# Optimization experiments

Measured on AMD Instinct MI355X. Metric: run time of the kernel, lower is better.

## Reference

```python
import jax, jax.numpy as jnp
import numpy as np

DIM = 384
HEADS = 6
HIDDEN = int(DIM * 4.0)
EPS = 1e-6

def setup_inputs() -> dict:
    key = jax.random.key(0)
    ks = jax.random.split(key, 8)
    s = 0.02
    return {
        "x": jax.random.normal(ks[0], (4, 2048, DIM), dtype=jnp.float32),
        "w_qkv": jax.random.normal(ks[1], (DIM, 3 * DIM), dtype=jnp.float32) * s,
        "b_qkv": jnp.zeros((3 * DIM,), dtype=jnp.float32),
        "w_proj": jax.random.normal(ks[2], (DIM, DIM), dtype=jnp.float32) * s,
        "b_proj": jnp.zeros((DIM,), dtype=jnp.float32),
        "w_fc1": jax.random.normal(ks[3], (DIM, HIDDEN), dtype=jnp.float32) * s,
        "b_fc1": jnp.zeros((HIDDEN,), dtype=jnp.float32),
        "w_fc2": jax.random.normal(ks[4], (HIDDEN, DIM), dtype=jnp.float32) * s,
        "b_fc2": jnp.zeros((DIM,), dtype=jnp.float32),
        "g1": jnp.ones((DIM,), dtype=jnp.float32),
        "beta1": jnp.zeros((DIM,), dtype=jnp.float32),
        "g2": jnp.ones((DIM,), dtype=jnp.float32),
        "beta2": jnp.zeros((DIM,), dtype=jnp.float32),
    }

def _layernorm(x, g, b):
    mu = jnp.mean(x, axis=-1, keepdims=True)
    var = jnp.mean(jnp.square(x - mu), axis=-1, keepdims=True)
    return (x - mu) * jax.lax.rsqrt(var + EPS) * g + b

def _attention(x, w_qkv, b_qkv, w_proj, b_proj):
    B, N, C = x.shape
    H = HEADS
    Dh = C // H
    qkv = x @ w_qkv + b_qkv                      # [B,N,3C]
    qkv = qkv.reshape(B, N, 3, H, Dh)
    q = jnp.transpose(qkv[:, :, 0], (0, 2, 1, 3))  # [B,H,N,Dh]
    k = jnp.transpose(qkv[:, :, 1], (0, 2, 1, 3))
    v = jnp.transpose(qkv[:, :, 2], (0, 2, 1, 3))
    scale = Dh ** -0.5
    attn = jnp.einsum('bhnd,bhmd->bhnm', q, k) * scale
    attn = jax.nn.softmax(attn, axis=-1)
    out = jnp.einsum('bhnm,bhmd->bhnd', attn, v)
    out = jnp.transpose(out, (0, 2, 1, 3)).reshape(B, N, C)
    return out @ w_proj + b_proj

def _mlp(x, w_fc1, b_fc1, w_fc2, b_fc2):
    h = jax.nn.gelu(x @ w_fc1 + b_fc1, approximate=False)
    return h @ w_fc2 + b_fc2

def reference(x, w_qkv, b_qkv, w_proj, b_proj, w_fc1, b_fc1, w_fc2, b_fc2, g1, beta1, g2, beta2):
    x = x + _attention(_layernorm(x, g1, beta1), w_qkv, b_qkv, w_proj, b_proj)
    x = x + _mlp(_layernorm(x, g2, beta2), w_fc1, b_fc1, w_fc2, b_fc2)
    return x
```

## Files before the change

kernel.cpp:

```cpp
#include <hip/hip_runtime.h>
#include <hip/hip_bf16.h>

#define TOK 8192
#define CDIM 384
#define HEADS 6
#define DH 64
#define HID 1536
#define SEQ 2048

#define QSCALE 0.18033688011112042f

typedef short bf16x8 __attribute__((ext_vector_type(8)));
typedef short bf16x4 __attribute__((ext_vector_type(4)));
typedef float f32x4 __attribute__((ext_vector_type(4)));
typedef float f32x16 __attribute__((ext_vector_type(16)));
typedef void __attribute__((address_space(1))) GV;
typedef void __attribute__((address_space(3))) SV;

#if __has_builtin(__builtin_amdgcn_exp2f)
#define EXP2(x) __builtin_amdgcn_exp2f(x)
#else
#define EXP2(x) exp2f(x)
#endif

__device__ __forceinline__ short f2bf(float f) {
    __hip_bfloat16 h = __float2bfloat16(f);
    return *reinterpret_cast<short*>(&h);
}

__device__ __forceinline__ int cvt_pk_bf16(float lo, float hi) {
    int r;
    asm("v_cvt_pk_bf16_f32 %0, %1, %2" : "=v"(r) : "v"(lo), "v"(hi));
    return r;
}

__device__ __forceinline__ void gl_lds16(const short* g, short* lds) {
    __builtin_amdgcn_global_load_lds((GV*)g, (SV*)lds, 16, 0, 0);
}

__device__ __forceinline__ float gelu_fast(float v) {
    const float A = 2.3022067f;
    const float B = 0.1029442f;
    const float u = v * (A + B * v * v);
    return v - v / (1.0f + EXP2(u));
}

__global__ __launch_bounds__(128) void ln_trans(const float* __restrict__ x,
                                                const float* __restrict__ g,
                                                const float* __restrict__ bta,
                                                short* __restrict__ y,
                                                const float* __restrict__ w_qkv,
                                                const float* __restrict__ w_proj,
                                                const float* __restrict__ w_fc1,
                                                const float* __restrict__ w_fc2,
                                                short* __restrict__ qkvT,
                                                short* __restrict__ projT,
                                                short* __restrict__ fc1T,
                                                short* __restrict__ fc2T) {
    if (blockIdx.x < TOK) {
        const int row = blockIdx.x;
        const float* xr = x + (size_t)row * CDIM;
        const int t = threadIdx.x;
        float v0 = xr[t], v1 = xr[t + 128], v2 = xr[t + 256];
        float s = v0 + v1 + v2;
        float ss = v0 * v0 + v1 * v1 + v2 * v2;
#pragma unroll
        for (int off = 1; off < 64; off <<= 1) {
            s += __shfl_xor(s, off);
            ss += __shfl_xor(ss, off);
        }
        __shared__ float sh[4];
        const int wv = t >> 6;
        if ((t & 63) == 0) { sh[wv] = s; sh[2 + wv] = ss; }
        __syncthreads();
        s = sh[0] + sh[1];
        ss = sh[2] + sh[3];
        const float mu = s * (1.0f / CDIM);
        const float var = ss * (1.0f / CDIM) - mu * mu;
        const float rs = rsqrtf(var + 1e-6f);
        short* yr = y + (size_t)row * CDIM;
        yr[t]       = f2bf((v0 - mu) * rs * g[t]       + bta[t]);
        yr[t + 128] = f2bf((v1 - mu) * rs * g[t + 128] + bta[t + 128]);
        yr[t + 256] = f2bf((v2 - mu) * rs * g[t + 256] + bta[t + 256]);
        return;
    }
    int b = blockIdx.x - TOK;
    const float* w; short* o; int K, N, nb;
    if (b < 432)       { w = w_qkv;  o = qkvT;  K = 384;  N = 1152; nb = 36; }
    else if (b < 576)  { b -= 432;  w = w_proj; o = projT; K = 384;  N = 384;  nb = 12; }
    else if (b < 1152) { b -= 576;  w = w_fc1;  o = fc1T;  K = 384;  N = 1536; nb = 48; }
    else               { b -= 1152; w = w_fc2;  o = fc2T;  K = 1536; N = 384;  nb = 12; }
    const int bx = (b % nb) * 32, by = (b / nb) * 32;
    __shared__ float t[32][33];
    const int tx = threadIdx.x & 31, ty = threadIdx.x >> 5;
#pragma unroll
    for (int i = 0; i < 8; ++i)
        t[ty + i * 4][tx] = w[(size_t)(by + ty + i * 4) * N + bx + tx];
    __syncthreads();
#pragma unroll
    for (int i = 0; i < 8; ++i)
        o[(size_t)(bx + ty + i * 4) * K + by + tx] = f2bf(t[tx][ty + i * 4]);
}

__global__ __launch_bounds__(128) void ln_kernel(const float* __restrict__ x,
                                                 const float* __restrict__ g,
                                                 const float* __restrict__ bta,
                                                 short* __restrict__ y) {
    const int row = blockIdx.x;
    const float* xr = x + (size_t)row * CDIM;
    const int t = threadIdx.x;
    float v0 = xr[t], v1 = xr[t + 128], v2 = xr[t + 256];
    float s = v0 + v1 + v2;
    float ss = v0 * v0 + v1 * v1 + v2 * v2;
#pragma unroll
    for (int off = 1; off < 64; off <<= 1) {
        s += __shfl_xor(s, off);
        ss += __shfl_xor(ss, off);
    }
    __shared__ float sh[4];
    const int wv = t >> 6;
    if ((t & 63) == 0) { sh[wv] = s; sh[2 + wv] = ss; }
    __syncthreads();
    s = sh[0] + sh[1];
    ss = sh[2] + sh[3];
    const float mu = s * (1.0f / CDIM);
    const float var = ss * (1.0f / CDIM) - mu * mu;
    const float rs = rsqrtf(var + 1e-6f);
    short* yr = y + (size_t)row * CDIM;
    yr[t]       = f2bf((v0 - mu) * rs * g[t]       + bta[t]);
    yr[t + 128] = f2bf((v1 - mu) * rs * g[t + 128] + bta[t + 128]);
    yr[t + 256] = f2bf((v2 - mu) * rs * g[t + 256] + bta[t + 256]);
}

template <int MODE, int MT>
__global__ __launch_bounds__(256) void mfma_gemm(const short* __restrict__ A,
                                                 const short* __restrict__ WT,
                                                 const float* __restrict__ bias,
                                                 const float* __restrict__ resid,
                                                 float* __restrict__ outF,
                                                 short* __restrict__ outB,
                                                 short* __restrict__ qb,
                                                 short* __restrict__ kb,
                                                 short* __restrict__ vtb,
                                                 int M, int N, int K) {
    constexpr int BN = (MT == 4) ? 128 : 64;
    constexpr int BM = (MT == 1) ? 64 : 128;
    constexpr int BUFS = (MT == 1) ? 3 : 1;
    __shared__ __align__(16) short As[BUFS * BM * 64];
    __shared__ __align__(16) short Bs[BUFS * BN * 64];

    const int tid  = threadIdx.x;
    const int w    = tid >> 6;
    const int lane = tid & 63;
    const int quad = lane >> 4;
    const int n15  = lane & 15;
    const int wr   = (MT == 4) ? (w >> 1) : w;
    const int wc   = (MT == 4) ? (w & 1) : 0;
    const int m0   = blockIdx.y * BM;
    const int n0   = blockIdx.x * BN;
    const int swz  = n15 & 7;

    f32x4 acc[MT][4];
#pragma unroll
    for (int i = 0; i < MT; ++i)
#pragma unroll
        for (int j = 0; j < 4; ++j) {
            acc[i][j][0] = 0; acc[i][j][1] = 0; acc[i][j][2] = 0; acc[i][j][3] = 0;
        }

    if constexpr (MT == 1) {
        const int nk = K >> 6;
#define STAGE1(buf, k0)                                                        \
    {                                                                          \
        short* Ad = As + (buf) * 4096;                                         \
        short* Bd = Bs + (buf) * 4096;                                         \
        _Pragma("unroll")                                                      \
        for (int i = 0; i < 2; ++i) {                                          \
            const int c = i * 256 + tid;                                       \
            const int r = c >> 3, p = c & 7;                                   \
            gl_lds16(A + (size_t)(m0 + r) * K + (k0) + ((p ^ (r & 7)) * 8),    \
                     Ad + (i * 256 + w * 64) * 8);                             \
        }                                                                      \
        _Pragma("unroll")                                                      \
        for (int i = 0; i < 2; ++i) {                                          \
            const int c = i * 256 + tid;                                       \
            const int r = c >> 3, p = c & 7;                                   \
            gl_lds16(WT + (size_t)(n0 + r) * K + (k0) + ((p ^ (r & 7)) * 8),   \
                     Bd + (i * 256 + w * 64) * 8);                             \
        }                                                                      \
    }
#define COMPUTE1(buf)                                                          \
    {                                                                          \
        const short* Ab = As + (buf) * 4096;                                   \
        const short* Bb = Bs + (buf) * 4096;                                   \
        _Pragma("unroll")                                                      \
        for (int kk = 0; kk < 2; ++kk) {                                       \
            bf16x8 af = *(const bf16x8*)&Ab[(w * 16 + n15) * 64 +              \
                                            (((kk * 4 + quad) ^ swz) * 8)];    \
            bf16x8 bfr[4];                                                     \
            _Pragma("unroll")                                                  \
            for (int nt = 0; nt < 4; ++nt)                                     \
                bfr[nt] = *(const bf16x8*)&Bb[(nt * 16 + n15) * 64 +           \
                                              (((kk * 4 + quad) ^ swz) * 8)];  \
            _Pragma("unroll")                                                  \
            for (int nt = 0; nt < 4; ++nt)                                     \
                acc[0][nt] = __builtin_amdgcn_mfma_f32_16x16x32_bf16(          \
                    af, bfr[nt], acc[0][nt], 0, 0, 0);                         \
        }                                                                      \
    }
        STAGE1(0, 0);
        STAGE1(1, 64);
        int cb = 0, sb = 2;
        for (int ks = 0; ks < nk; ++ks) {
            __builtin_amdgcn_s_barrier();
            if (ks + 2 < nk) {
                STAGE1(sb, (ks + 2) << 6);
                asm volatile("s_waitcnt vmcnt(8)" ::: "memory");
            } else if (ks + 1 < nk) {
                asm volatile("s_waitcnt vmcnt(4)" ::: "memory");
            } else {
                asm volatile("s_waitcnt vmcnt(0)" ::: "memory");
            }
            __builtin_amdgcn_s_barrier();
            COMPUTE1(cb);
            cb = (cb == 2) ? 0 : cb + 1;
            sb = (sb == 2) ? 0 : sb + 1;
        }
#undef STAGE1
#undef COMPUTE1
    } else {
        for (int k0 = 0; k0 < K; k0 += 64) {
            __syncthreads();
#pragma unroll
            for (int i = 0; i < BM / 32; ++i) {
                const int c = i * 256 + tid;
                const int r = c >> 3, p = c & 7;
                gl_lds16(A + (size_t)(m0 + r) * K + k0 + ((p ^ (r & 7)) * 8),
                         As + (i * 256 + w * 64) * 8);
            }
#pragma unroll
            for (int i = 0; i < BN / 32; ++i) {
                const int c = i * 256 + tid;
                const int r = c >> 3, p = c & 7;
                gl_lds16(WT + (size_t)(n0 + r) * K + k0 + ((p ^ (r & 7)) * 8),
                         Bs + (i * 256 + w * 64) * 8);
            }
            __syncthreads();

#pragma unroll
            for (int kk = 0; kk < 2; ++kk) {
                bf16x8 af[MT], bfr[4];
#pragma unroll
                for (int mt = 0; mt < MT; ++mt)
                    af[mt] = *(const bf16x8*)&As[(wr * (MT * 16) + mt * 16 + n15) * 64 +
                                                 (((kk * 4 + quad) ^ swz) * 8)];
#pragma unroll
                for (int nt = 0; nt < 4; ++nt)
                    bfr[nt] = *(const bf16x8*)&Bs[(wc * 64 + nt * 16 + n15) * 64 +
                                                  (((kk * 4 + quad) ^ swz) * 8)];
#pragma unroll
                for (int mt = 0; mt < MT; ++mt)
#pragma unroll
                    for (int nt = 0; nt < 4; ++nt)
                        acc[mt][nt] = __builtin_amdgcn_mfma_f32_16x16x32_bf16(af[mt], bfr[nt], acc[mt][nt], 0, 0, 0);
            }
        }
    }

#pragma unroll
    for (int nt = 0; nt < 4; ++nt) {
        const int col = n0 + wc * 64 + nt * 16 + n15;
        const float bv = bias[col];
        if constexpr (MODE == 2) {
            const int part = col / CDIM;
            const int rem  = col - part * CDIM;
            const int h    = rem >> 6;
            const int d    = rem & 63;
#pragma unroll
            for (int mt = 0; mt < MT; ++mt) {
                const int r0 = m0 + wr * (MT * 16) + mt * 16 + quad * 4;
                const int bi = r0 >> 11;
                const int n  = r0 & 2047;
                if (part == 2) {
                    short4 pkv;
                    pkv.x = f2bf(acc[mt][nt][0] + bv);
                    pkv.y = f2bf(acc[mt][nt][1] + bv);
                    pkv.z = f2bf(acc[mt][nt][2] + bv);
                    pkv.w = f2bf(acc[mt][nt][3] + bv);
                    *(short4*)&vtb[((size_t)(bi * HEADS + h) * DH + d) * SEQ + n] = pkv;
                } else {
                    short* dst = (part == 0 ? qb : kb) +
                                 ((size_t)(bi * HEADS + h) * SEQ + n) * DH + d;
#pragma unroll
                    for (int rr = 0; rr < 4; ++rr) {
                        float o = acc[mt][nt][rr] + bv;
                        if (part == 0) o *= QSCALE;
                        dst[(size_t)rr * DH] = f2bf(o);
                    }
                }
            }
        } else {
#pragma unroll
            for (int mt = 0; mt < MT; ++mt)
#pragma unroll
                for (int rr = 0; rr < 4; ++rr) {
                    const int r = m0 + wr * (MT * 16) + mt * 16 + quad * 4 + rr;
                    float o = acc[mt][nt][rr] + bv;
                    if constexpr (MODE == 1) {
                        outB[(size_t)r * N + col] = f2bf(gelu_fast(o));
                    } else {
                        if (resid) o += resid[(size_t)r * N + col];
                        outF[(size_t)r * N + col] = o;
                    }
                }
        }
    }
}

__global__ __launch_bounds__(256, 4) void attn_mfma(const short* __restrict__ qb,
                                                    const short* __restrict__ kb,
                                                    const short* __restrict__ vtb,
                                                    short* __restrict__ outp) {
    __shared__ __align__(16) char smem[33792];

    const int bid = blockIdx.x;
    const int x   = bid & 7;
    const int j   = bid >> 3;
    const int bh  = x * 3 + (j >> 6);
    const int qt  = j & 63;
    const int bi  = bh / HEADS;
    const int h   = bh - bi * HEADS;

    const int tid  = threadIdx.x;
    const int w    = tid >> 6;
    const int lane = tid & 63;
    const int l31  = lane & 31;
    const int hi   = lane >> 5;

    short* Kl  = (short*)(smem + w * 8192);
    short* Vtl = (short*)(smem + w * 8192 + 4096);

    const size_t headoff = (size_t)bh * SEQ * DH;

    bf16x8 qf[4];
    {
        const short* qg = qb + headoff + (size_t)(qt * 32 + l31) * DH + hi * 8;
#pragma unroll
        for (int kc = 0; kc < 4; ++kc)
            qf[kc] = *(const bf16x8*)(qg + kc * 16);
    }
    asm volatile("s_waitcnt vmcnt(0)" ::: "memory");

    const int l3 = lane >> 3, l7 = lane & 7;
    const int l2 = lane >> 2, p4 = lane & 3;
    const short* kg = kb + headoff + (size_t)(w * 32 + l3) * DH + ((l7 ^ l3) * 8);
    const short* vg = vtb + (size_t)bh * DH * SEQ + (size_t)l2 * SEQ +
                      ((p4 ^ (l2 & 3)) * 8) + w * 32;

    const int swk = l31 & 7;
    const int swv = l31 & 3;
    const int krd = l31 * 64;
    const int vrd = l31 * 32;

    f32x16 O0 = {}, O1 = {}, Lc = {};
    const f32x16 Zc = {};

    bf16x8 ones;
    {
        const short one = 0x3F80;
#pragma unroll
        for (int i = 0; i < 8; ++i) ones[i] = one;
    }

#define STAGE_K(tt) { const short* kgt = kg + (size_t)(tt) * 128 * DH;             \
        _Pragma("unroll") for (int i = 0; i < 4; ++i)                              \
            gl_lds16(kgt + i * 512, Kl + i * 512); }
#define STAGE_V(tt) { const short* vgt = vg + (tt) * 128;                          \
        _Pragma("unroll") for (int i = 0; i < 4; ++i)                              \
            gl_lds16(vgt + (size_t)i * 16 * SEQ, Vtl + i * 512); }

    STAGE_K(0);
    STAGE_V(0);

    for (int t = 0; t < SEQ / 128; ++t) {
        asm volatile("s_waitcnt vmcnt(4)" ::: "memory");
        __builtin_amdgcn_sched_barrier(0);

        bf16x8 kf0 = *(const bf16x8*)&Kl[krd + (((0 + hi) ^ swk) * 8)];
        bf16x8 kf1 = *(const bf16x8*)&Kl[krd + (((2 + hi) ^ swk) * 8)];
        bf16x8 kf2 = *(const bf16x8*)&Kl[krd + (((4 + hi) ^ swk) * 8)];
        bf16x8 kf3 = *(const bf16x8*)&Kl[krd + (((6 + hi) ^ swk) * 8)];
        asm volatile("s_waitcnt lgkmcnt(0)" ::: "memory");
        __builtin_amdgcn_sched_barrier(0);
        if (t < SEQ / 128 - 1) STAGE_K(t + 1);

        f32x16 S = __builtin_amdgcn_mfma_f32_32x32x16_bf16(kf0, qf[0], Zc, 0, 0, 0);
        S = __builtin_amdgcn_mfma_f32_32x32x16_bf16(kf1, qf[1], S, 0, 0, 0);
        S = __builtin_amdgcn_mfma_f32_32x32x16_bf16(kf2, qf[2], S, 0, 0, 0);
        S = __builtin_amdgcn_mfma_f32_32x32x16_bf16(kf3, qf[3], S, 0, 0, 0);

        if (t < SEQ / 128 - 1) {
            asm volatile("s_waitcnt vmcnt(4)" ::: "memory");
        } else {
            asm volatile("s_waitcnt vmcnt(0)" ::: "memory");
        }
        __builtin_amdgcn_sched_barrier(0);

        bf16x8 v00 = *(const bf16x8*)&Vtl[vrd + ((hi ^ swv) * 8)];
        bf16x8 v01 = *(const bf16x8*)&Vtl[vrd + (((2 + hi) ^ swv) * 8)];
        bf16x8 v10 = *(const bf16x8*)&Vtl[1024 + vrd + ((hi ^ swv) * 8)];
        bf16x8 v11 = *(const bf16x8*)&Vtl[1024 + vrd + (((2 + hi) ^ swv) * 8)];
        asm volatile("s_waitcnt lgkmcnt(0)" ::: "memory");
        __builtin_amdgcn_sched_barrier(0);
        if (t < SEQ / 128 - 1) STAGE_V(t + 1);

        float e[16];
#pragma unroll
        for (int r = 0; r < 16; ++r) e[r] = EXP2(S[r]);

        int p0 = cvt_pk_bf16(e[0], e[1]),   p1 = cvt_pk_bf16(e[2], e[3]);
        int p2 = cvt_pk_bf16(e[4], e[5]),   p3 = cvt_pk_bf16(e[6], e[7]);
        asm("v_permlane32_swap_b32 %0, %1" : "+v"(p0), "+v"(p2));
        asm("v_permlane32_swap_b32 %0, %1" : "+v"(p1), "+v"(p3));
        int p4w = cvt_pk_bf16(e[8], e[9]),  p5 = cvt_pk_bf16(e[10], e[11]);
        int p6 = cvt_pk_bf16(e[12], e[13]), p7 = cvt_pk_bf16(e[14], e[15]);
        asm("v_permlane32_swap_b32 %0, %1" : "+v"(p4w), "+v"(p6));
        asm("v_permlane32_swap_b32 %0, %1" : "+v"(p5), "+v"(p7));
        bf16x8 pf0, pf1;
        { int pw[4] = {p0, p1, p2, p3};   __builtin_memcpy(&pf0, pw, 16); }
        { int pw[4] = {p4w, p5, p6, p7};  __builtin_memcpy(&pf1, pw, 16); }

        O0 = __builtin_amdgcn_mfma_f32_32x32x16_bf16(v00, pf0, O0, 0, 0, 0);
        O0 = __builtin_amdgcn_mfma_f32_32x32x16_bf16(v01, pf1, O0, 0, 0, 0);
        O1 = __builtin_amdgcn_mfma_f32_32x32x16_bf16(v10, pf0, O1, 0, 0, 0);
        O1 = __builtin_amdgcn_mfma_f32_32x32x16_bf16(v11, pf1, O1, 0, 0, 0);
        Lc = __builtin_amdgcn_mfma_f32_32x32x16_bf16(ones, pf0, Lc, 0, 0, 0);
        Lc = __builtin_amdgcn_mfma_f32_32x32x16_bf16(ones, pf1, Lc, 0, 0, 0);
    }
#undef STAGE_K
#undef STAGE_V

    __syncthreads();
    float* Obuf = (float*)smem;
    float* lbuf = (float*)(smem + 33280);
    float* myO  = Obuf + w * 2080;
#pragma unroll
    for (int r = 0; r < 16; ++r) {
        const int d0 = (r & 3) + 8 * (r >> 2) + 4 * hi;
        myO[l31 * 65 + d0]      = O0[r];
        myO[l31 * 65 + 32 + d0] = O1[r];
    }
    if (hi == 0) lbuf[w * 32 + l31] = Lc[0];
    __syncthreads();

    const int quad = lane >> 4;
    const int n15  = lane & 15;
    const int d = w * 16 + n15;
#pragma unroll
    for (int i = 0; i < 8; ++i) {
        const int q = quad * 8 + i;
        const float l = lbuf[q] + lbuf[32 + q] + lbuf[64 + q] + lbuf[96 + q];
        const float s = Obuf[q * 65 + d] + Obuf[2080 + q * 65 + d] +
                        Obuf[4160 + q * 65 + d] + Obuf[6240 + q * 65 + d];
        outp[(size_t)(bi * SEQ + qt * 32 + q) * CDIM + h * DH + d] = f2bf(s / l);
    }
}

extern "C" void kernel_launch(void* const* d_in, const int* in_sizes, int n_in,
                              void* d_out, int out_size, void* d_ws, size_t ws_size,
                              hipStream_t stream) {
    const float* x      = (const float*)d_in[0];
    const float* w_qkv  = (const float*)d_in[1];
    const float* b_qkv  = (const float*)d_in[2];
    const float* w_proj = (const float*)d_in[3];
    const float* b_proj = (const float*)d_in[4];
    const float* w_fc1  = (const float*)d_in[5];
    const float* b_fc1  = (const float*)d_in[6];
    const float* w_fc2  = (const float*)d_in[7];
    const float* b_fc2  = (const float*)d_in[8];
    const float* g1     = (const float*)d_in[9];
    const float* beta1  = (const float*)d_in[10];
    const float* g2     = (const float*)d_in[11];
    const float* beta2  = (const float*)d_in[12];
    float* out = (float*)d_out;

    short* qkvT = (short*)d_ws;
    short* projT = qkvT + 1152 * 384;
    short* fc1T  = projT + 384 * 384;
    short* fc2T  = fc1T + 1536 * 384;
    short* y     = fc2T + 384 * 1536;
    short* qb    = y + (size_t)TOK * 384;
    short* kb    = qb + (size_t)TOK * 384;
    short* vtb   = kb + (size_t)TOK * 384;
    short* attn  = vtb + (size_t)TOK * 384;
    short* hbuf  = attn + (size_t)TOK * 384;

    ln_trans<<<TOK + 1728, 128, 0, stream>>>(x, g1, beta1, y,
                                             w_qkv, w_proj, w_fc1, w_fc2,
                                             qkvT, projT, fc1T, fc2T);
    mfma_gemm<2, 4><<<dim3(1152 / 128, TOK / 128), 256, 0, stream>>>(
        y, qkvT, b_qkv, nullptr, nullptr, nullptr, qb, kb, vtb, TOK, 3 * CDIM, CDIM);
    attn_mfma<<<1536, 256, 0, stream>>>(qb, kb, vtb, attn);
    mfma_gemm<0, 1><<<dim3(CDIM / 64, TOK / 64), 256, 0, stream>>>(
        attn, projT, b_proj, x, out, nullptr, nullptr, nullptr, nullptr, TOK, CDIM, CDIM);
    ln_kernel<<<TOK, 128, 0, stream>>>(out, g2, beta2, y);
    mfma_gemm<1, 4><<<dim3(HID / 128, TOK / 128), 256, 0, stream>>>(
        y, fc1T, b_fc1, nullptr, nullptr, hbuf, nullptr, nullptr, nullptr, TOK, HID, CDIM);
    mfma_gemm<0, 1><<<dim3(CDIM / 64, TOK / 64), 256, 0, stream>>>(
        hbuf, fc2T, b_fc2, out, out, nullptr, nullptr, nullptr, nullptr, TOK, CDIM, HID);
}
```

Before: 227.9 us.

## Process two 32-query tiles per attention block to reuse K/V staging

Each attention block now handles 64 queries, as two 32-row query tiles, instead of 32, and the grid is halved to 768 blocks. The K and V tiles staged into LDS and loaded into registers are reused for both query tiles, which halves global K/V traffic and LDS reads per query. The cost is roughly double the accumulator registers (O and L for both tiles), which may hurt occupancy under launch_bounds(256,4). The epilogue also becomes two sequential LDS reduction passes.

Result: slower. 475.6 us (+108.7%).

```diff
diff --git a/kernel.cpp b/kernel.cpp
--- a/kernel.cpp
+++ b/kernel.cpp
@@ -326,8 +326,8 @@
     const int bid = blockIdx.x;
     const int x   = bid & 7;
     const int j   = bid >> 3;
-    const int bh  = x * 3 + (j >> 6);
-    const int qt  = j & 63;
+    const int bh  = x * 3 + (j >> 5);
+    const int qt  = j & 31;
     const int bi  = bh / HEADS;
     const int h   = bh - bi * HEADS;
 
@@ -342,12 +342,18 @@
 
     const size_t headoff = (size_t)bh * SEQ * DH;
 
-    bf16x8 qf[4];
+    bf16x8 qf00, qf01, qf02, qf03, qf10, qf11, qf12, qf13;
     {
-        const short* qg = qb + headoff + (size_t)(qt * 32 + l31) * DH + hi * 8;
-#pragma unroll
-        for (int kc = 0; kc < 4; ++kc)
-            qf[kc] = *(const bf16x8*)(qg + kc * 16);
+        const short* qg0 = qb + headoff + (size_t)(qt * 64 + l31) * DH + hi * 8;
+        const short* qg1 = qg0 + 32 * DH;
+        qf00 = *(const bf16x8*)(qg0);
+        qf01 = *(const bf16x8*)(qg0 + 16);
+        qf02 = *(const bf16x8*)(qg0 + 32);
+        qf03 = *(const bf16x8*)(qg0 + 48);
+        qf10 = *(const bf16x8*)(qg1);
+        qf11 = *(const bf16x8*)(qg1 + 16);
+        qf12 = *(const bf16x8*)(qg1 + 32);
+        qf13 = *(const bf16x8*)(qg1 + 48);
     }
     asm volatile("s_waitcnt vmcnt(0)" ::: "memory");
 
@@ -362,7 +368,7 @@
     const int krd = l31 * 64;
     const int vrd = l31 * 32;
 
-    f32x16 O0 = {}, O1 = {}, Lc = {};
+    f32x16 O00 = {}, O01 = {}, O10 = {}, O11 = {}, Lc0 = {}, Lc1 = {};
     const f32x16 Zc = {};
 
     bf16x8 ones;
@@ -394,10 +400,14 @@
         __builtin_amdgcn_sched_barrier(0);
         if (t < SEQ / 128 - 1) STAGE_K(t + 1);
 
-        f32x16 S = __builtin_amdgcn_mfma_f32_32x32x16_bf16(kf0, qf[0], Zc, 0, 0, 0);
-        S = __builtin_amdgcn_mfma_f32_32x32x16_bf16(kf1, qf[1], S, 0, 0, 0);
-        S = __builtin_amdgcn_mfma_f32_32x32x16_bf16(kf2, qf[2], S, 0, 0, 0);
-        S = __builtin_amdgcn_mfma_f32_32x32x16_bf16(kf3, qf[3], S, 0, 0, 0);
+        f32x16 S0 = __builtin_amdgcn_mfma_f32_32x32x16_bf16(kf0, qf00, Zc, 0, 0, 0);
+        S0 = __builtin_amdgcn_mfma_f32_32x32x16_bf16(kf1, qf01, S0, 0, 0, 0);
+        S0 = __builtin_amdgcn_mfma_f32_32x32x16_bf16(kf2, qf02, S0, 0, 0, 0);
+        S0 = __builtin_amdgcn_mfma_f32_32x32x16_bf16(kf3, qf03, S0, 0, 0, 0);
+        f32x16 S1 = __builtin_amdgcn_mfma_f32_32x32x16_bf16(kf0, qf10, Zc, 0, 0, 0);
+        S1 = __builtin_amdgcn_mfma_f32_32x32x16_bf16(kf1, qf11, S1, 0, 0, 0);
+        S1 = __builtin_amdgcn_mfma_f32_32x32x16_bf16(kf2, qf12, S1, 0, 0, 0);
+        S1 = __builtin_amdgcn_mfma_f32_32x32x16_bf16(kf3, qf13, S1, 0, 0, 0);
 
         if (t < SEQ / 128 - 1) {
             asm volatile("s_waitcnt vmcnt(4)" ::: "memory");
@@ -414,55 +424,96 @@
         __builtin_amdgcn_sched_barrier(0);
         if (t < SEQ / 128 - 1) STAGE_V(t + 1);
 
-        float e[16];
-#pragma unroll
-        for (int r = 0; r < 16; ++r) e[r] = EXP2(S[r]);
-
-        int p0 = cvt_pk_bf16(e[0], e[1]),   p1 = cvt_pk_bf16(e[2], e[3]);
-        int p2 = cvt_pk_bf16(e[4], e[5]),   p3 = cvt_pk_bf16(e[6], e[7]);
-        asm("v_permlane32_swap_b32 %0, %1" : "+v"(p0), "+v"(p2));
-        asm("v_permlane32_swap_b32 %0, %1" : "+v"(p1), "+v"(p3));
-        int p4w = cvt_pk_bf16(e[8], e[9]),  p5 = cvt_pk_bf16(e[10], e[11]);
-        int p6 = cvt_pk_bf16(e[12], e[13]), p7 = cvt_pk_bf16(e[14], e[15]);
-        asm("v_permlane32_swap_b32 %0, %1" : "+v"(p4w), "+v"(p6));
-        asm("v_permlane32_swap_b32 %0, %1" : "+v"(p5), "+v"(p7));
-        bf16x8 pf0, pf1;
-        { int pw[4] = {p0, p1, p2, p3};   __builtin_memcpy(&pf0, pw, 16); }
-        { int pw[4] = {p4w, p5, p6, p7};  __builtin_memcpy(&pf1, pw, 16); }
-
-        O0 = __builtin_amdgcn_mfma_f32_32x32x16_bf16(v00, pf0, O0, 0, 0, 0);
-        O0 = __builtin_amdgcn_mfma_f32_32x32x16_bf16(v01, pf1, O0, 0, 0, 0);
-        O1 = __builtin_amdgcn_mfma_f32_32x32x16_bf16(v10, pf0, O1, 0, 0, 0);
-        O1 = __builtin_amdgcn_mfma_f32_32x32x16_bf16(v11, pf1, O1, 0, 0, 0);
-        Lc = __builtin_amdgcn_mfma_f32_32x32x16_bf16(ones, pf0, Lc, 0, 0, 0);
-        Lc = __builtin_amdgcn_mfma_f32_32x32x16_bf16(ones, pf1, Lc, 0, 0, 0);
+        bf16x8 pf00, pf01;
+        {
+            float e[16];
+#pragma unroll
+            for (int r = 0; r < 16; ++r) e[r] = EXP2(S0[r]);
+            int p0 = cvt_pk_bf16(e[0], e[1]),   p1 = cvt_pk_bf16(e[2], e[3]);
+            int p2 = cvt_pk_bf16(e[4], e[5]),   p3 = cvt_pk_bf16(e[6], e[7]);
+            asm("v_permlane32_swap_b32 %0, %1" : "+v"(p0), "+v"(p2));
+            asm("v_permlane32_swap_b32 %0, %1" : "+v"(p1), "+v"(p3));
+            int p4w = cvt_pk_bf16(e[8], e[9]),  p5 = cvt_pk_bf16(e[10], e[11]);
+            int p6 = cvt_pk_bf16(e[12], e[13]), p7 = cvt_pk_bf16(e[14], e[15]);
+            asm("v_permlane32_swap_b32 %0, %1" : "+v"(p4w), "+v"(p6));
+            asm("v_permlane32_swap_b32 %0, %1" : "+v"(p5), "+v"(p7));
+            { int pw[4] = {p0, p1, p2, p3};   __builtin_memcpy(&pf00, pw, 16); }
+            { int pw[4] = {p4w, p5, p6, p7};  __builtin_memcpy(&pf01, pw, 16); }
+        }
+        bf16x8 pf10, pf11;
+        {
+            float e[16];
+#pragma unroll
+            for (int r = 0; r < 16; ++r) e[r] = EXP2(S1[r]);
+            int p0 = cvt_pk_bf16(e[0], e[1]),   p1 = cvt_pk_bf16(e[2], e[3]);
+            int p2 = cvt_pk_bf16(e[4], e[5]),   p3 = cvt_pk_bf16(e[6], e[7]);
+            asm("v_permlane32_swap_b32 %0, %1" : "+v"(p0), "+v"(p2));
+            asm("v_permlane32_swap_b32 %0, %1" : "+v"(p1), "+v"(p3));
+            int p4w = cvt_pk_bf16(e[8], e[9]),  p5 = cvt_pk_bf16(e[10], e[11]);
+            int p6 = cvt_pk_bf16(e[12], e[13]), p7 = cvt_pk_bf16(e[14], e[15]);
+            asm("v_permlane32_swap_b32 %0, %1" : "+v"(p4w), "+v"(p6));
+            asm("v_permlane32_swap_b32 %0, %1" : "+v"(p5), "+v"(p7));
+            { int pw[4] = {p0, p1, p2, p3};   __builtin_memcpy(&pf10, pw, 16); }
+            { int pw[4] = {p4w, p5, p6, p7};  __builtin_memcpy(&pf11, pw, 16); }
+        }
+
+        O00 = __builtin_amdgcn_mfma_f32_32x32x16_bf16(v00, pf00, O00, 0, 0, 0);
+        O00 = __builtin_amdgcn_mfma_f32_32x32x16_bf16(v01, pf01, O00, 0, 0, 0);
+        O01 = __builtin_amdgcn_mfma_f32_32x32x16_bf16(v10, pf00, O01, 0, 0, 0);
+        O01 = __builtin_amdgcn_mfma_f32_32x32x16_bf16(v11, pf01, O01, 0, 0, 0);
+        Lc0 = __builtin_amdgcn_mfma_f32_32x32x16_bf16(ones, pf00, Lc0, 0, 0, 0);
+        Lc0 = __builtin_amdgcn_mfma_f32_32x32x16_bf16(ones, pf01, Lc0, 0, 0, 0);
+        O10 = __builtin_amdgcn_mfma_f32_32x32x16_bf16(v00, pf10, O10, 0, 0, 0);
+        O10 = __builtin_amdgcn_mfma_f32_32x32x16_bf16(v01, pf11, O10, 0, 0, 0);
+        O11 = __builtin_amdgcn_mfma_f32_32x32x16_bf16(v10, pf10, O11, 0, 0, 0);
+        O11 = __builtin_amdgcn_mfma_f32_32x32x16_bf16(v11, pf11, O11, 0, 0, 0);
+        Lc1 = __builtin_amdgcn_mfma_f32_32x32x16_bf16(ones, pf10, Lc1, 0, 0, 0);
+        Lc1 = __builtin_amdgcn_mfma_f32_32x32x16_bf16(ones, pf11, Lc1, 0, 0, 0);
     }
 #undef STAGE_K
 #undef STAGE_V
 
-    __syncthreads();
     float* Obuf = (float*)smem;
     float* lbuf = (float*)(smem + 33280);
     float* myO  = Obuf + w * 2080;
-#pragma unroll
-    for (int r = 0; r < 16; ++r) {
-        const int d0 = (r & 3) + 8 * (r >> 2) + 4 * hi;
-        myO[l31 * 65 + d0]      = O0[r];
-        myO[l31 * 65 + 32 + d0] = O1[r];
-    }
-    if (hi == 0) lbuf[w * 32 + l31] = Lc[0];
-    __syncthreads();
-
     const int quad = lane >> 4;
     const int n15  = lane & 15;
     const int d = w * 16 + n15;
+
+    __syncthreads();
+#pragma unroll
+    for (int r = 0; r < 16; ++r) {
+        const int d0 = (r & 3) + 8 * (r >> 2) + 4 * hi;
+        myO[l31 * 65 + d0]      = O00[r];
+        myO[l31 * 65 + 32 + d0] = O01[r];
+    }
+    if (hi == 0) lbuf[w * 32 + l31] = Lc0[0];
+    __syncthreads();
 #pragma unroll
     for (int i = 0; i < 8; ++i) {
         const int q = quad * 8 + i;
         const float l = lbuf[q] + lbuf[32 + q] + lbuf[64 + q] + lbuf[96 + q];
         const float s = Obuf[q * 65 + d] + Obuf[2080 + q * 65 + d] +
                         Obuf[4160 + q * 65 + d] + Obuf[6240 + q * 65 + d];
-        outp[(size_t)(bi * SEQ + qt * 32 + q) * CDIM + h * DH + d] = f2bf(s / l);
+        outp[(size_t)(bi * SEQ + qt * 64 + q) * CDIM + h * DH + d] = f2bf(s / l);
+    }
+
+    __syncthreads();
+#pragma unroll
+    for (int r = 0; r < 16; ++r) {
+        const int d0 = (r & 3) + 8 * (r >> 2) + 4 * hi;
+        myO[l31 * 65 + d0]      = O10[r];
+        myO[l31 * 65 + 32 + d0] = O11[r];
+    }
+    if (hi == 0) lbuf[w * 32 + l31] = Lc1[0];
+    __syncthreads();
+#pragma unroll
+    for (int i = 0; i < 8; ++i) {
+        const int q = quad * 8 + i;
+        const float l = lbuf[q] + lbuf[32 + q] + lbuf[64 + q] + lbuf[96 + q];
+        const float s = Obuf[q * 65 + d] + Obuf[2080 + q * 65 + d] +
+                        Obuf[4160 + q * 65 + d] + Obuf[6240 + q * 65 + d];
+        outp[(size_t)(bi * SEQ + qt * 64 + 32 + q) * CDIM + h * DH + d] = f2bf(s / l);
     }
 }
 
@@ -500,7 +551,7 @@
                                              qkvT, projT, fc1T, fc2T);
     mfma_gemm<2, 4><<<dim3(1152 / 128, TOK / 128), 256, 0, stream>>>(
         y, qkvT, b_qkv, nullptr, nullptr, nullptr, qb, kb, vtb, TOK, 3 * CDIM, CDIM);
-    attn_mfma<<<1536, 256, 0, stream>>>(qb, kb, vtb, attn);
+    attn_mfma<<<768, 256, 0, stream>>>(qb, kb, vtb, attn);
     mfma_gemm<0, 1><<<dim3(CDIM / 64, TOK / 64), 256, 0, stream>>>(
         attn, projT, b_proj, x, out, nullptr, nullptr, nullptr, nullptr, TOK, CDIM, CDIM);
     ln_kernel<<<TOK, 128, 0, stream>>>(out, g2, beta2, y);
```

## Use split-K across warps for FC2 GEMM with LDS reduction

Applied to the files above, without the earlier changes.

Replaces the generic 64x64 MFMA GEMM for the FC2 projection (K=1536) with a dedicated kernel in which each of the four warps handles a quarter of K on the full 64x64 tile. Each warp double-buffers its own LDS slab, with no block-wide barriers in the main loop. The four partial sums are then reduced through shared memory and added to the bias and residual. The aim is to cut inter-warp synchronisation and raise per-warp MFMA density, at the cost of 64KB of LDS per block, which lowers occupancy, plus an extra reduction pass.

New measurement: 228.1 us. No clear change (+0.1%).

```diff
diff --git a/kernel.cpp b/kernel.cpp
--- a/kernel.cpp
+++ b/kernel.cpp
@@ -317,6 +317,104 @@
     }
 }
 
+__global__ __launch_bounds__(256) void gemm_wp_fc2(const short* __restrict__ A,
+                                                   const short* __restrict__ WT,
+                                                   const float* __restrict__ bias,
+                                                   float* __restrict__ outF) {
+    __shared__ __align__(16) char smem[65536];
+    const int K = HID, N = CDIM;
+
+    const int tid  = threadIdx.x;
+    const int w    = tid >> 6;
+    const int lane = tid & 63;
+    const int quad = lane >> 4;
+    const int n15  = lane & 15;
+    const int swz  = n15 & 7;
+    const int m0   = blockIdx.y * 64;
+    const int n0   = blockIdx.x * 64;
+
+    short* Aw = (short*)(smem + w * 16384);
+    short* Bw = Aw + 4096;
+
+    const int l3 = lane >> 3, l7 = lane & 7;
+    const int kw = w * (K / 4);
+    const short* Ag = A  + (size_t)(m0 + l3) * K + kw + ((l7 ^ l3) * 8);
+    const short* Bg = WT + (size_t)(n0 + l3) * K + kw + ((l7 ^ l3) * 8);
+
+#define STAGE_WP(ks)                                                           \
+    {                                                                          \
+        const short* Agt = Ag + (ks) * 64;                                     \
+        const short* Bgt = Bg + (ks) * 64;                                     \
+        _Pragma("unroll")                                                      \
+        for (int ld = 0; ld < 8; ++ld) {                                       \
+            gl_lds16(Agt + (size_t)ld * 8 * K, Aw + ld * 512);                 \
+            gl_lds16(Bgt + (size_t)ld * 8 * K, Bw + ld * 512);                 \
+        }                                                                      \
+    }
+
+    f32x4 acc[4][4];
+#pragma unroll
+    for (int i = 0; i < 4; ++i)
+#pragma unroll
+        for (int j = 0; j < 4; ++j) {
+            acc[i][j][0] = 0; acc[i][j][1] = 0; acc[i][j][2] = 0; acc[i][j][3] = 0;
+        }
+
+    STAGE_WP(0);
+
+    for (int ks = 0; ks < 6; ++ks) {
+        asm volatile("s_waitcnt vmcnt(0)" ::: "memory");
+        __builtin_amdgcn_sched_barrier(0);
+
+        bf16x8 af[2][4], bfr[2][4];
+#pragma unroll
+        for (int kk = 0; kk < 2; ++kk)
+#pragma unroll
+            for (int t4 = 0; t4 < 4; ++t4) {
+                af[kk][t4]  = *(const bf16x8*)&Aw[(t4 * 16 + n15) * 64 +
+                                                  (((kk * 4 + quad) ^ swz) * 8)];
+                bfr[kk][t4] = *(const bf16x8*)&Bw[(t4 * 16 + n15) * 64 +
+                                                  (((kk * 4 + quad) ^ swz) * 8)];
+            }
+        asm volatile("s_waitcnt lgkmcnt(0)" ::: "memory");
+        __builtin_amdgcn_sched_barrier(0);
+        if (ks + 1 < 6) STAGE_WP(ks + 1);
+
+#pragma unroll
+        for (int kk = 0; kk < 2; ++kk)
+#pragma unroll
+            for (int mt = 0; mt < 4; ++mt)
+#pragma unroll
+                for (int nt = 0; nt < 4; ++nt)
+                    acc[mt][nt] = __builtin_amdgcn_mfma_f32_16x16x32_bf16(
+                        af[kk][mt], bfr[kk][nt], acc[mt][nt], 0, 0, 0);
+    }
+#undef STAGE_WP
+
+    __syncthreads();
+    float* P = (float*)smem;
+    float* myP = P + w * 4096;
+#pragma unroll
+    for (int mt = 0; mt < 4; ++mt)
+#pragma unroll
+        for (int nt = 0; nt < 4; ++nt)
+#pragma unroll
+            for (int rr = 0; rr < 4; ++rr)
+                myP[(mt * 16 + quad * 4 + rr) * 64 + nt * 16 + n15] = acc[mt][nt][rr];
+    __syncthreads();
+
+    const int r  = tid >> 2;
+    const int c0 = (tid & 3) * 16;
+#pragma unroll
+    for (int c = 0; c < 16; ++c) {
+        const int cc = c0 + c;
+        const float s = P[r * 64 + cc] + P[4096 + r * 64 + cc] +
+                        P[8192 + r * 64 + cc] + P[12288 + r * 64 + cc];
+        const size_t idx = (size_t)(m0 + r) * N + n0 + cc;
+        outF[idx] = outF[idx] + s + bias[n0 + cc];
+    }
+}
+
 __global__ __launch_bounds__(256, 4) void attn_mfma(const short* __restrict__ qb,
                                                     const short* __restrict__ kb,
                                                     const short* __restrict__ vtb,
@@ -506,6 +604,5 @@
     ln_kernel<<<TOK, 128, 0, stream>>>(out, g2, beta2, y);
     mfma_gemm<1, 4><<<dim3(HID / 128, TOK / 128), 256, 0, stream>>>(
         y, fc1T, b_fc1, nullptr, nullptr, hbuf, nullptr, nullptr, nullptr, TOK, HID, CDIM);
-    mfma_gemm<0, 1><<<dim3(CDIM / 64, TOK / 64), 256, 0, stream>>>(
-        hbuf, fc2T, b_fc2, out, out, nullptr, nullptr, nullptr, nullptr, TOK, CDIM, HID);
-}
+    gemm_wp_fc2<<<dim3(CDIM / 64, TOK / 64), 256, 0, stream>>>(hbuf, fc2T, b_fc2, out);
+}
```
